# Optimization experiments

Hardware: AMD Instinct MI355X
Metric: run time of the kernel (lower is better)

Reference implementation:

```python
import jax, jax.numpy as jnp
import numpy as np


def setup_inputs() -> dict:
    key = jax.random.key(0)
    # qkv: [B, 3*C, T] with B=32 (batch*heads), C=64 head channels, T=2048 tokens
    qkv = jax.random.normal(key, (32, 192, 2048), dtype=jnp.float32)
    return {"qkv": qkv}


def reference(qkv):
    channel = qkv.shape[1] // 3
    q, k, v = jnp.split(qkv, 3, axis=1)  # each [B, C, T]
    scale = 1.0 / np.sqrt(np.sqrt(channel))  # applied to both q and k (total 1/sqrt(C))
    # scores: [B, T, S]
    attn_score = jnp.einsum('bct,bcs->bts', q * scale, k * scale)
    attn_score = jax.nn.softmax(attn_score.astype(jnp.float32), axis=-1).astype(attn_score.dtype)
    # output: [B, C, T]
    return jnp.einsum('bts,bcs->bct', attn_score, v)
```

## Files before the change

### kernel.cpp

```cpp
#include <hip/hip_runtime.h>

#define B_ 32
#define C_ 64
#define T_ 2048
#define TM 128
#define TN 64
#define LDB 144

typedef __bf16 bf16x8 __attribute__((ext_vector_type(8)));
typedef float f32x4 __attribute__((ext_vector_type(4)));

__device__ __forceinline__ unsigned short f2bf(float x) {
  unsigned int u = __float_as_uint(x);
  u += 0x7fffu + ((u >> 16) & 1u);
  return (unsigned short)(u >> 16);
}

__device__ __forceinline__ unsigned cvtpk(float lo, float hi) {
  unsigned r;
  asm("v_cvt_pk_bf16_f32 %0, %1, %2" : "=v"(r) : "v"(lo), "v"(hi));
  return r;
}

__device__ __forceinline__ int swz(int row, int col) {
  return row * LDB + ((((col >> 3) ^ (row >> 3)) & 7) << 4) + ((col & 7) << 1);
}

__global__ __launch_bounds__(256) void attn_swapped(const float* __restrict__ qkv,
                                                    float* __restrict__ out) {
  __shared__ __align__(16) char smem[2][2][64 * LDB];

  const int tid = threadIdx.x;
  const int b = blockIdx.y;
  const int t0 = blockIdx.x * TM;
  const float* qb = qkv + (size_t)b * (3 * C_ * T_);
  const float* kb = qb + C_ * T_;
  const float* vb = qb + 2 * C_ * T_;
  const float scale = 0.3535533905932738f;

  const int l = tid & 63;
  const int w = tid >> 6;
  const int lr = l & 15;
  const int lh = l >> 4;
  const int t0w = t0 + w * 32;

  bf16x8 qf[2][2];
#pragma unroll
  for (int tq = 0; tq < 2; ++tq)
#pragma unroll
    for (int h = 0; h < 2; ++h) {
      float qv[8];
#pragma unroll
      for (int j = 0; j < 8; ++j)
        qv[j] = qb[(size_t)(h * 32 + lh * 8 + j) * T_ + t0w + tq * 16 + lr] * scale;
      union { unsigned u[4]; bf16x8 v; } tmp;
#pragma unroll
      for (int j = 0; j < 4; ++j) tmp.u[j] = cvtpk(qv[2 * j], qv[2 * j + 1]);
      qf[tq][h] = tmp.v;
    }

  const int sq = (tid & 15) * 4;
  const int cr = tid >> 4;

  auto stage = [&](int s0, int d) {
    char* Kb = smem[d][0];
    char* Vb = smem[d][1];
#pragma unroll
    for (int i = 0; i < 4; ++i) {
      const int c = cr + i * 16;
      const float4 kv = *(const float4*)(kb + (size_t)c * T_ + s0 + sq);
      *(unsigned short*)(Kb + swz(sq + 0, c)) = f2bf(kv.x * scale);
      *(unsigned short*)(Kb + swz(sq + 1, c)) = f2bf(kv.y * scale);
      *(unsigned short*)(Kb + swz(sq + 2, c)) = f2bf(kv.z * scale);
      *(unsigned short*)(Kb + swz(sq + 3, c)) = f2bf(kv.w * scale);
      const float4 vv = *(const float4*)(vb + (size_t)c * T_ + s0 + sq);
      uint2 vp;
      vp.x = cvtpk(vv.x, vv.y);
      vp.y = cvtpk(vv.z, vv.w);
      *(uint2*)(Vb + swz(c, sq)) = vp;
    }
  };

  f32x4 o[4][2];
#pragma unroll
  for (int cf = 0; cf < 4; ++cf)
#pragma unroll
    for (int tq = 0; tq < 2; ++tq) o[cf][tq] = (f32x4){0.f, 0.f, 0.f, 0.f};
  float psum[2] = {0.f, 0.f};

  stage(0, 0);
  __syncthreads();

  for (int it = 0; it < T_ / TN; ++it) {
    const int d = it & 1;
    if (it + 1 < T_ / TN) stage((it + 1) * TN, d ^ 1);

    const char* Kb = smem[d][0];
    const char* Vb = smem[d][1];

    f32x4 sc[2][4];
#pragma unroll
    for (int ns = 0; ns < 4; ++ns) {
      const int srow = ns * 16 + lr;
      const int rb = srow * LDB;
      const int sl = (srow >> 3) & 7;
      const bf16x8 k0 = *(const bf16x8*)(Kb + rb + (((lh ^ sl) & 7) << 4));
      const bf16x8 k1 = *(const bf16x8*)(Kb + rb + ((((lh + 4) ^ sl) & 7) << 4));
#pragma unroll
      for (int tq = 0; tq < 2; ++tq) {
        f32x4 acc = (f32x4){0.f, 0.f, 0.f, 0.f};
        acc = __builtin_amdgcn_mfma_f32_16x16x32_bf16(k0, qf[tq][0], acc, 0, 0, 0);
        acc = __builtin_amdgcn_mfma_f32_16x16x32_bf16(k1, qf[tq][1], acc, 0, 0, 0);
        sc[tq][ns] = acc;
      }
    }

    unsigned pd[2][2][4];
#pragma unroll
    for (int tq = 0; tq < 2; ++tq) {
      float ps = 0.f;
#pragma unroll
      for (int ns = 0; ns < 4; ++ns) {
        f32x4 pv;
#pragma unroll
        for (int r = 0; r < 4; ++r) {
          pv[r] = __expf(sc[tq][ns][r]);
          ps += pv[r];
        }
        pd[tq][ns >> 1][(ns & 1) * 2 + 0] = cvtpk(pv[0], pv[1]);
        pd[tq][ns >> 1][(ns & 1) * 2 + 1] = cvtpk(pv[2], pv[3]);
      }
      psum[tq] += ps;
    }

#pragma unroll
    for (int cf = 0; cf < 4; ++cf) {
      const int crow = cf * 16 + lr;
#pragma unroll
      for (int m = 0; m < 2; ++m) {
        const int s1 = m * 32 + lh * 4;
        union { uint2 q[2]; bf16x8 v; } vf;
        vf.q[0] = *(const uint2*)(Vb + swz(crow, s1));
        vf.q[1] = *(const uint2*)(Vb + swz(crow, s1 + 16));
        union { unsigned u[4]; bf16x8 v; } pf0, pf1;
#pragma unroll
        for (int j = 0; j < 4; ++j) { pf0.u[j] = pd[0][m][j]; pf1.u[j] = pd[1][m][j]; }
        o[cf][0] = __builtin_amdgcn_mfma_f32_16x16x32_bf16(vf.v, pf0.v, o[cf][0], 0, 0, 0);
        o[cf][1] = __builtin_amdgcn_mfma_f32_16x16x32_bf16(vf.v, pf1.v, o[cf][1], 0, 0, 0);
      }
    }
    __syncthreads();
  }

  float inv[2];
#pragma unroll
  for (int tq = 0; tq < 2; ++tq) {
    float s = psum[tq];
    s += __shfl_xor(s, 16, 64);
    s += __shfl_xor(s, 32, 64);
    inv[tq] = 1.0f / s;
  }
  float* ob = out + (size_t)b * (C_ * T_);
#pragma unroll
  for (int cf = 0; cf < 4; ++cf)
#pragma unroll
    for (int tq = 0; tq < 2; ++tq)
#pragma unroll
      for (int r = 0; r < 4; ++r)
        ob[(size_t)(cf * 16 + lh * 4 + r) * T_ + t0w + tq * 16 + lr] = o[cf][tq][r] * inv[tq];
}

extern "C" void kernel_launch(void* const* d_in, const int* in_sizes, int n_in,
                              void* d_out, int out_size, void* d_ws, size_t ws_size,
                              hipStream_t stream) {
  const float* qkv = (const float*)d_in[0];
  float* out = (float*)d_out;
  dim3 grid(T_ / TM, B_);
  dim3 block(256);
  hipLaunchKernelGGL(attn_swapped, grid, block, 0, stream, qkv, out);
}
```

Measured before the change: 74.49 us.

## Split K/V staging into register prefetch and deferred LDS write, use exp2

```diff
diff --git a/kernel.cpp b/kernel.cpp
--- a/kernel.cpp
+++ b/kernel.cpp
@@ -10,15 +10,15 @@
 typedef __bf16 bf16x8 __attribute__((ext_vector_type(8)));
 typedef float f32x4 __attribute__((ext_vector_type(4)));
 
-__device__ __forceinline__ unsigned short f2bf(float x) {
-  unsigned int u = __float_as_uint(x);
-  u += 0x7fffu + ((u >> 16) & 1u);
-  return (unsigned short)(u >> 16);
-}
-
 __device__ __forceinline__ unsigned cvtpk(float lo, float hi) {
   unsigned r;
   asm("v_cvt_pk_bf16_f32 %0, %1, %2" : "=v"(r) : "v"(lo), "v"(hi));
+  return r;
+}
+
+__device__ __forceinline__ float exp2v(float x) {
+  float r;
+  asm("v_exp_f32 %0, %1" : "=v"(r) : "v"(x));
   return r;
 }
 
@@ -36,7 +36,7 @@
   const float* qb = qkv + (size_t)b * (3 * C_ * T_);
   const float* kb = qb + C_ * T_;
   const float* vb = qb + 2 * C_ * T_;
-  const float scale = 0.3535533905932738f;
+  const float qscale = 0.18033688011112042f;
 
   const int l = tid & 63;
   const int w = tid >> 6;
@@ -52,32 +52,40 @@
       float qv[8];
 #pragma unroll
       for (int j = 0; j < 8; ++j)
-        qv[j] = qb[(size_t)(h * 32 + lh * 8 + j) * T_ + t0w + tq * 16 + lr] * scale;
+        qv[j] = qb[(size_t)(h * 32 + lh * 8 + j) * T_ + t0w + tq * 16 + lr] * qscale;
       union { unsigned u[4]; bf16x8 v; } tmp;
 #pragma unroll
       for (int j = 0; j < 4; ++j) tmp.u[j] = cvtpk(qv[2 * j], qv[2 * j + 1]);
       qf[tq][h] = tmp.v;
     }
 
-  const int sq = (tid & 15) * 4;
-  const int cr = tid >> 4;
+  const int cb = (tid >> 4) * 4;
+  const int sq4 = (tid & 15) * 4;
 
-  auto stage = [&](int s0, int d) {
+  f32x4 kreg[4], vreg[4];
+  auto loadKV = [&](int s0) {
+#pragma unroll
+    for (int i = 0; i < 4; ++i) {
+      kreg[i] = *(const f32x4*)(kb + (size_t)(cb + i) * T_ + s0 + sq4);
+      vreg[i] = *(const f32x4*)(vb + (size_t)(cb + i) * T_ + s0 + sq4);
+    }
+  };
+  auto writeKV = [&](int d) {
     char* Kb = smem[d][0];
     char* Vb = smem[d][1];
 #pragma unroll
+    for (int j = 0; j < 4; ++j) {
+      uint2 u;
+      u.x = cvtpk(kreg[0][j], kreg[1][j]);
+      u.y = cvtpk(kreg[2][j], kreg[3][j]);
+      *(uint2*)(Kb + swz(sq4 + j, cb)) = u;
+    }
+#pragma unroll
     for (int i = 0; i < 4; ++i) {
-      const int c = cr + i * 16;
-      const float4 kv = *(const float4*)(kb + (size_t)c * T_ + s0 + sq);
-      *(unsigned short*)(Kb + swz(sq + 0, c)) = f2bf(kv.x * scale);
-      *(unsigned short*)(Kb + swz(sq + 1, c)) = f2bf(kv.y * scale);
-      *(unsigned short*)(Kb + swz(sq + 2, c)) = f2bf(kv.z * scale);
-      *(unsigned short*)(Kb + swz(sq + 3, c)) = f2bf(kv.w * scale);
-      const float4 vv = *(const float4*)(vb + (size_t)c * T_ + s0 + sq);
-      uint2 vp;
-      vp.x = cvtpk(vv.x, vv.y);
-      vp.y = cvtpk(vv.z, vv.w);
-      *(uint2*)(Vb + swz(c, sq)) = vp;
+      uint2 u;
+      u.x = cvtpk(vreg[i][0], vreg[i][1]);
+      u.y = cvtpk(vreg[i][2], vreg[i][3]);
+      *(uint2*)(Vb + swz(cb + i, sq4)) = u;
     }
   };
 
@@ -88,12 +96,15 @@
     for (int tq = 0; tq < 2; ++tq) o[cf][tq] = (f32x4){0.f, 0.f, 0.f, 0.f};
   float psum[2] = {0.f, 0.f};
 
-  stage(0, 0);
+  loadKV(0);
+  writeKV(0);
   __syncthreads();
 
-  for (int it = 0; it < T_ / TN; ++it) {
+  const int NT = T_ / TN;
+  for (int it = 0; it < NT; ++it) {
     const int d = it & 1;
-    if (it + 1 < T_ / TN) stage((it + 1) * TN, d ^ 1);
+    const bool pf = (it + 1 < NT);
+    if (pf) loadKV((it + 1) * TN);
 
     const char* Kb = smem[d][0];
     const char* Vb = smem[d][1];
@@ -124,7 +135,7 @@
         f32x4 pv;
 #pragma unroll
         for (int r = 0; r < 4; ++r) {
-          pv[r] = __expf(sc[tq][ns][r]);
+          pv[r] = exp2v(sc[tq][ns][r]);
           ps += pv[r];
         }
         pd[tq][ns >> 1][(ns & 1) * 2 + 0] = cvtpk(pv[0], pv[1]);
@@ -132,6 +143,8 @@
       }
       psum[tq] += ps;
     }
+
+    if (pf) writeKV(d ^ 1);
 
 #pragma unroll
     for (int cf = 0; cf < 4; ++cf) {
```

Result: faster. 64.80 us (-13.0%).
